# Kernel optimization log

Measured on AMD Instinct MI355X. Metric: run time of the kernel, lower is better.

The kernel has to match this reference:

```python
import jax, jax.numpy as jnp
import numpy as np
from jax import lax

B, S, C = 32, 64, 512      # batch, source length, context dim
E, H, L = 256, 512, 2      # embed dim, hidden dim, num GRU layers
V = 32000                  # vocab
START = 1                  # start token index


def setup_inputs() -> dict:
    key = jax.random.key(0)
    ks = jax.random.split(key, 16)
    s = 0.02
    d = {
        'context': jax.random.normal(ks[0], (B, S, C), jnp.float32),
        'max_len': 32,
        'embed': (jax.random.normal(ks[1], (V, E), jnp.float32) * s),
        'Wa': jax.random.normal(ks[2], (1, C + H), jnp.float32) * s,
        'ba': jnp.zeros((1,), jnp.float32),
        # GRU layer 0: input = E + C
        'W_ih0': jax.random.normal(ks[3], (3 * H, E + C), jnp.float32) * s,
        'W_hh0': jax.random.normal(ks[4], (3 * H, H), jnp.float32) * s,
        'b_ih0': jnp.zeros((3 * H,), jnp.float32),
        'b_hh0': jnp.zeros((3 * H,), jnp.float32),
        # GRU layer 1: input = H
        'W_ih1': jax.random.normal(ks[5], (3 * H, H), jnp.float32) * s,
        'W_hh1': jax.random.normal(ks[6], (3 * H, H), jnp.float32) * s,
        'b_ih1': jnp.zeros((3 * H,), jnp.float32),
        'b_hh1': jnp.zeros((3 * H,), jnp.float32),
        'Wo': jax.random.normal(ks[7], (V, H), jnp.float32) * s,
        'bo': jnp.zeros((V,), jnp.float32),
    }
    return d


def _gru_cell(x, h, Wih, Whh, bih, bhh):
    # PyTorch GRUCell math: gates order (r, z, n)
    gx = x @ Wih.T + bih
    gh = h @ Whh.T + bhh
    rx, zx, nx = jnp.split(gx, 3, axis=-1)
    rh, zh, nh = jnp.split(gh, 3, axis=-1)
    r = jax.nn.sigmoid(rx + rh)
    z = jax.nn.sigmoid(zx + zh)
    n = jnp.tanh(nx + r * nh)
    return (1.0 - z) * n + z * h


def reference(context, max_len, embed, Wa, ba,
              W_ih0, W_hh0, b_ih0, b_hh0,
              W_ih1, W_hh1, b_ih1, b_hh1,
              Wo, bo):
    def step(carry, _):
        x, hid = carry                      # x: [B] int32, hid: [L,B,H]
        ex = embed[x]                       # [B,E]
        htop = hid[L - 1]                   # [B,H] (top layer hidden)
        mem = jnp.broadcast_to(htop[:, None, :], (B, S, H))
        score = jnp.tanh(jnp.concatenate([mem, context], -1) @ Wa.T + ba)[..., 0]  # [B,S]
        w = jax.nn.softmax(score, axis=1)   # attention weights over source
        attend = jnp.einsum('bs,bsc->bc', w, context)  # [B,C]
        inp = jnp.concatenate([ex, attend], -1)        # [B,E+C]
        h0 = _gru_cell(inp, hid[0], W_ih0, W_hh0, b_ih0, b_hh0)
        h1 = _gru_cell(h0, hid[1], W_ih1, W_hh1, b_ih1, b_hh1)
        logp = jax.nn.log_softmax(h1 @ Wo.T + bo, axis=-1)  # [B,V]
        x_next = jnp.argmax(logp, axis=-1).astype(jnp.int32)  # greedy (detached)
        return (x_next, jnp.stack([h0, h1])), (logp, w)

    x0 = jnp.full((B,), START, jnp.int32)
    h0 = jnp.zeros((L, B, H), context.dtype)
    _, (outs, atts) = lax.scan(step, (x0, h0), None, length=max_len)
    out = jnp.transpose(outs, (1, 0, 2))        # [B,max_len,V]
    attention = jnp.transpose(atts, (1, 0, 2))  # [B,max_len,S]
    return out, attention
```

## Files before the change

kernel.cpp:

```cpp
#include <hip/hip_runtime.h>

#define B_ 32
#define S_ 64
#define C_ 512
#define E_ 256
#define H_ 512
#define V_ 32000
#define T_ 32
#define NTHR 512
#define ND 250
#define START_TOK 1
#define DELTA 0.05f
#define BH (B_ * H_)

#define OFF_CS   0
#define OFF_LSEA 2048
#define OFF_A2V  3072
#define OFF_A2I  527360
#define OFF_LSM  1051648
#define OFF_LSS  1313792
#define OFF_ATT  1575936
#define OFF_H0   1592320
#define OFF_H1   1625088
#define OFF_H1BF 1657856
#define OFF_WOBF 1920000
#define OFF_SYNC 10112000
#define WS_FLOATS 10113024

typedef unsigned long long ull;
typedef __attribute__((ext_vector_type(8))) short bf16x8;
typedef __attribute__((ext_vector_type(4))) float f32x4;

struct Params {
  const float* ctx; const float* embed; const float* Wa;
  const float* Wih0; const float* Whh0; const float* bih0; const float* bhh0;
  const float* Wih1; const float* Whh1; const float* bih1; const float* bhh1;
  const float* Wo; const float* bo;
  float* ws; float* out;
};

__device__ __forceinline__ float sigf(float x) { return 1.0f / (1.0f + expf(-x)); }

__device__ __forceinline__ unsigned short f2bf(float f) {
  unsigned u = __builtin_bit_cast(unsigned, f);
  unsigned r = (u + 0x7FFFu + ((u >> 16) & 1u)) >> 16;
  return (unsigned short)r;
}

__device__ __forceinline__ void lse_merge(float& m, float& s, float m2, float s2) {
  float M = fmaxf(m, m2);
  s = s * expf(m - M) + s2 * expf(m2 - M);
  m = M;
}

__device__ __forceinline__ void st_cf(float* p, float v) {
  __hip_atomic_store(p, v, __ATOMIC_RELAXED, __HIP_MEMORY_SCOPE_AGENT);
}
__device__ __forceinline__ unsigned ld_cu(const unsigned* p) {
  return __hip_atomic_load(p, __ATOMIC_RELAXED, __HIP_MEMORY_SCOPE_AGENT);
}

__global__ void __launch_bounds__(256) zero_k(float* wsf) {
  const unsigned i = blockIdx.x * 256u + threadIdx.x;
  if (i < 524288u) {
    wsf[OFF_A2V + i] = -3.0e38f;
    ((int*)wsf)[OFF_A2I + i] = 0x7fffffff;
  }
  if (i < 65536u) wsf[OFF_H0 + i] = 0.0f;
  if (i < 1024u) ((unsigned*)wsf)[OFF_SYNC + i] = 0u;
}

__global__ void __launch_bounds__(256) cscore_k(const float* __restrict__ ctx,
                                                const float* __restrict__ Wa,
                                                const float* __restrict__ ba,
                                                float* __restrict__ wsf) {
  const int b = blockIdx.x;
  const int s = threadIdx.x >> 2, q = threadIdx.x & 3;
  const float* cp = ctx + ((size_t)b * S_ + s) * C_ + q * 128;
  const float* wp = Wa + H_ + q * 128;
  float acc = 0.f;
#pragma unroll 8
  for (int k = 0; k < 128; ++k) acc = fmaf(cp[k], wp[k], acc);
  acc += __shfl_xor(acc, 1);
  acc += __shfl_xor(acc, 2);
  if (q == 0) wsf[OFF_CS + b * S_ + s] = acc + ba[0];
}

__global__ void __launch_bounds__(256) cvt_wobf(const float* __restrict__ wo,
                                                unsigned short* __restrict__ dst) {
  const size_t i = ((size_t)blockIdx.x * 256u + threadIdx.x) * 4;
  float4 v = *(const float4*)(wo + i);
  ushort4 o;
  o.x = f2bf(v.x); o.y = f2bf(v.y); o.z = f2bf(v.z); o.w = f2bf(v.w);
  *(ushort4*)(dst + i) = o;
}

__global__ void __launch_bounds__(NTHR) attn0_k(const float* __restrict__ ctx,
                                                float* __restrict__ wsf,
                                                float* __restrict__ out) {
  const int b = blockIdx.x, tx = threadIdx.x;
  __shared__ float wlds[S_];
  if (tx < S_) {
    float sc = tanhf(wsf[OFF_CS + b * S_ + tx]);
    float e = expf(sc); float sum = e;
#pragma unroll
    for (int d = 1; d < 64; d <<= 1) sum += __shfl_xor(sum, d);
    float w = e / sum; wlds[tx] = w;
    out[(size_t)B_ * T_ * V_ + ((size_t)b * T_ + 0) * S_ + tx] = w;
  }
  __syncthreads();
  float a0 = 0.f;
  const float* cb = ctx + (size_t)b * S_ * C_ + tx;
#pragma unroll 8
  for (int s2 = 0; s2 < S_; ++s2) a0 = fmaf(wlds[s2], cb[(size_t)s2 * C_], a0);
  wsf[OFF_ATT + (size_t)b * H_ + tx] = a0;
}

__global__ void __launch_bounds__(NTHR) k_gru01(Params p, int t) {
  float* wsf = p.ws;
  unsigned short* h1bf = (unsigned short*)(wsf + OFF_H1BF);
  const int bk = blockIdx.x, tx = threadIdx.x;
  const int ug = bk & 31, bg = bk >> 5, b4 = bg * 4;
  const int par = t & 1;
  __shared__ __align__(16) float sacts[4 * 768];
  __shared__ __align__(16) float sh0l[4 * 512];
  __shared__ __align__(16) float sh1r[4 * 512];
  __shared__ __align__(16) float sx[4 * 512];
  __shared__ int   stok4[4];
  __shared__ float scrV[8];
  __shared__ int   scrI[8];
  __shared__ float scrM[8];
  __shared__ int   slist4[4][16];
  __shared__ int   scnt4[4];
  __shared__ float hout[64];

  {
    const int bb = tx >> 7, cc = (tx & 127) * 4;
    float4 va = *(const float4*)(wsf + OFF_ATT + (size_t)(b4 + bb) * H_ + cc);
    float4 vh = *(const float4*)(wsf + OFF_H0 + (size_t)par * BH + (size_t)(b4 + bb) * H_ + cc);
    float4 vr = *(const float4*)(wsf + OFF_H1 + (size_t)par * BH + (size_t)(b4 + bb) * H_ + cc);
    *(float4*)&sacts[bb * 768 + 256 + cc] = va;
    *(float4*)&sh0l[bb * 512 + cc] = vh;
    *(float4*)&sh1r[bb * 512 + cc] = vr;
  }
  __syncthreads();
  if (t > 0) {
    const int w = tx >> 6, lane = tx & 63;
    const int lb = w >> 1, ws2 = w & 1, b = b4 + lb;
    const int gtx = tx & 127;
    const size_t cb_ = (size_t)(t - 1) * 32 + b;
    const float* avp = wsf + OFF_A2V + cb_ * 512;
    const int*   aip = (const int*)wsf + OFF_A2I + cb_ * 512;
    float v[4]; int id[4];
#pragma unroll
    for (int e = 0; e < 4; ++e) { v[e] = avp[gtx * 4 + e]; id[e] = aip[gtx * 4 + e]; }
    float M = fmaxf(fmaxf(v[0], v[1]), fmaxf(v[2], v[3]));
#pragma unroll
    for (int d = 1; d < 64; d <<= 1) M = fmaxf(M, __shfl_xor(M, d));
    if (lane == 0) scrM[w] = M;
    if (tx < 4) scnt4[tx] = 0;
    __syncthreads();
    M = fmaxf(scrM[lb * 2], scrM[lb * 2 + 1]);
#pragma unroll
    for (int e = 0; e < 4; ++e) {
      if (v[e] >= M - DELTA && id[e] != 0x7fffffff) {
        int k = atomicAdd(&scnt4[lb], 1);
        if (k < 16) slist4[lb][k] = id[e];
      }
    }
    __syncthreads();
    const int nc = min(scnt4[lb], 16);
    float bV = -3.0e38f; int bI = 0x7fffffff;
    for (int c = ws2; c < nc; c += 2) {
      const int idx = slist4[lb][c];
      const float* wr = p.Wo + (size_t)idx * H_ + lane * 8;
      const float* hr = sh1r + lb * 512 + lane * 8;
      float a = 0.f;
#pragma unroll
      for (int e = 0; e < 8; ++e) a = fmaf(hr[e], wr[e], a);
#pragma unroll
      for (int d = 1; d < 64; d <<= 1) a += __shfl_xor(a, d);
      a += p.bo[idx];
      if (a > bV || (a == bV && idx < bI)) { bV = a; bI = idx; }
    }
    if (lane == 0) { scrV[w] = bV; scrI[w] = bI; }
    __syncthreads();
    if (tx < 4) {
      float v0 = scrV[tx * 2], v1 = scrV[tx * 2 + 1];
      int i0 = scrI[tx * 2], i1 = scrI[tx * 2 + 1];
      stok4[tx] = (v1 > v0 || (v1 == v0 && i1 < i0)) ? i1 : i0;
    }
  } else {
    if (tx < 4) stok4[tx] = START_TOK;
  }
  __syncthreads();
#pragma unroll
  for (int k = 0; k < 2; ++k) {
    const int idx = k * NTHR + tx;
    const int bb = idx >> 8, e = idx & 255;
    sacts[bb * 768 + e] = p.embed[(size_t)stok4[bb] * E_ + e];
  }
  __syncthreads();
  const int u = tx >> 5, l = tx & 31;
  const int j = ug * 16 + u;
  {
    float red[16];
#pragma unroll
    for (int q = 0; q < 16; ++q) red[q] = 0.f;
#pragma unroll
    for (int g = 0; g < 3; ++g) {
      const float4* wx = (const float4*)(p.Wih0 + (size_t)(g * H_ + j) * 768);
      float* dx = (g < 2) ? &red[g * 4] : &red[8];
#pragma unroll
      for (int c = 0; c < 6; ++c) {
        float4 w = wx[l + 32 * c];
#pragma unroll
        for (int b2 = 0; b2 < 4; ++b2) {
          const float* a = &sacts[b2 * 768 + 4 * l + 128 * c];
          dx[b2] = fmaf(w.x, a[0], dx[b2]); dx[b2] = fmaf(w.y, a[1], dx[b2]);
          dx[b2] = fmaf(w.z, a[2], dx[b2]); dx[b2] = fmaf(w.w, a[3], dx[b2]);
        }
      }
      const float4* wh = (const float4*)(p.Whh0 + (size_t)(g * H_ + j) * H_);
      float* dh = (g < 2) ? &red[g * 4] : &red[12];
#pragma unroll
      for (int c = 0; c < 4; ++c) {
        float4 w = wh[l + 32 * c];
#pragma unroll
        for (int b2 = 0; b2 < 4; ++b2) {
          const float* a = &sh0l[b2 * 512 + 4 * l + 128 * c];
          dh[b2] = fmaf(w.x, a[0], dh[b2]); dh[b2] = fmaf(w.y, a[1], dh[b2]);
          dh[b2] = fmaf(w.z, a[2], dh[b2]); dh[b2] = fmaf(w.w, a[3], dh[b2]);
        }
      }
    }
#pragma unroll
    for (int d = 1; d < 32; d <<= 1)
#pragma unroll
      for (int q = 0; q < 16; ++q) red[q] += __shfl_xor(red[q], d);
    if (l < 4) {
      const float rr = sigf(red[l] + p.bih0[j] + p.bhh0[j]);
      const float zz = sigf(red[4 + l] + p.bih0[H_ + j] + p.bhh0[H_ + j]);
      const float nn = tanhf(red[8 + l] + p.bih0[2 * H_ + j] +
                             rr * (red[12 + l] + p.bhh0[2 * H_ + j]));
      const float hp = sh0l[l * 512 + j];
      st_cf(wsf + OFF_H0 + (size_t)(1 - par) * BH + (size_t)(b4 + l) * H_ + j,
            (1.f - zz) * nn + zz * hp);
    }
  }
  asm volatile("s_waitcnt vmcnt(0)" ::: "memory");
  __syncthreads();
  {
    unsigned* cnt = (unsigned*)wsf + OFF_SYNC + bg * 128 + t;
    if (tx == 0) {
      __hip_atomic_fetch_add(cnt, 1u, __ATOMIC_RELAXED, __HIP_MEMORY_SCOPE_AGENT);
      while (ld_cu(cnt) < 32u) __builtin_amdgcn_s_sleep(1);
    }
  }
  __syncthreads();
  {
    const ull* pX = (const ull*)(wsf + OFF_H0 + (size_t)(1 - par) * BH);
    ull vx[2];
#pragma unroll
    for (int k = 0; k < 2; ++k) {
      const int iu = k * NTHR + tx;
      const int bb = iu >> 8, cc = iu & 255;
      const ull* a1 = pX + (size_t)(b4 + bb) * 256 + cc;
      asm volatile("global_load_dwordx2 %0, %1, off sc0 sc1" : "=v"(vx[k]) : "v"(a1));
    }
    asm volatile("s_waitcnt vmcnt(0)" ::: "memory");
#pragma unroll
    for (int k = 0; k < 2; ++k) {
      const int iu = k * NTHR + tx;
      const int bb = iu >> 8, cc = iu & 255;
      *(ull*)&sx[bb * 512 + cc * 2] = vx[k];
    }
  }
  __syncthreads();
  {
    float red[16];
#pragma unroll
    for (int q = 0; q < 16; ++q) red[q] = 0.f;
#pragma unroll
    for (int g = 0; g < 3; ++g) {
      const float4* wx = (const float4*)(p.Wih1 + (size_t)(g * H_ + j) * H_);
      float* dx = (g < 2) ? &red[g * 4] : &red[8];
#pragma unroll
      for (int c = 0; c < 4; ++c) {
        float4 w = wx[l + 32 * c];
#pragma unroll
        for (int b2 = 0; b2 < 4; ++b2) {
          const float* a = &sx[b2 * 512 + 4 * l + 128 * c];
          dx[b2] = fmaf(w.x, a[0], dx[b2]); dx[b2] = fmaf(w.y, a[1], dx[b2]);
          dx[b2] = fmaf(w.z, a[2], dx[b2]); dx[b2] = fmaf(w.w, a[3], dx[b2]);
        }
      }
      const float4* wh = (const float4*)(p.Whh1 + (size_t)(g * H_ + j) * H_);
      float* dh = (g < 2) ? &red[g * 4] : &red[12];
#pragma unroll
      for (int c = 0; c < 4; ++c) {
        float4 w = wh[l + 32 * c];
#pragma unroll
        for (int b2 = 0; b2 < 4; ++b2) {
          const float* a = &sh1r[b2 * 512 + 4 * l + 128 * c];
          dh[b2] = fmaf(w.x, a[0], dh[b2]); dh[b2] = fmaf(w.y, a[1], dh[b2]);
          dh[b2] = fmaf(w.z, a[2], dh[b2]); dh[b2] = fmaf(w.w, a[3], dh[b2]);
        }
      }
    }
#pragma unroll
    for (int d = 1; d < 32; d <<= 1)
#pragma unroll
      for (int q = 0; q < 16; ++q) red[q] += __shfl_xor(red[q], d);
    if (l < 4) {
      const float rr = sigf(red[l] + p.bih1[j] + p.bhh1[j]);
      const float zz = sigf(red[4 + l] + p.bih1[H_ + j] + p.bhh1[H_ + j]);
      const float nn = tanhf(red[8 + l] + p.bih1[2 * H_ + j] +
                             rr * (red[12 + l] + p.bhh1[2 * H_ + j]));
      const float hp = sh1r[l * 512 + j];
      const float hnew = (1.f - zz) * nn + zz * hp;
      wsf[OFF_H1 + (size_t)(1 - par) * BH + (size_t)(b4 + l) * H_ + j] = hnew;
      hout[u * 4 + l] = hnew;
    }
  }
  __syncthreads();
  if (tx < 32) {
    const int b2 = tx & 3, pp = tx >> 2;
    const float h0v = hout[(pp * 2) * 4 + b2];
    const float h1v = hout[(pp * 2 + 1) * 4 + b2];
    const unsigned pk = (unsigned)f2bf(h0v) | ((unsigned)f2bf(h1v) << 16);
    *(int*)(h1bf + ((size_t)t * B_ + b4 + b2) * H_ + ug * 16 + pp * 2) = (int)pk;
  }
}

__device__ __constant__ int AST[7] = {0, 6, 12, 17, 22, 27, 32};

__global__ void __launch_bounds__(NTHR) k_scan(Params p, int t) {
  float* wsf = p.ws;
  const unsigned short* h1bf = (const unsigned short*)(wsf + OFF_H1BF);
  const unsigned short* wobf = (const unsigned short*)(wsf + OFF_WOBF);
  const int bk = blockIdx.x, tx = threadIdx.x;
  const int par = t & 1;
  __shared__ float scrF[8][16][4];
  __shared__ int   scrI2[8][16][2];
  __shared__ float wlds[S_];
  __shared__ float shsS;
  __shared__ float rv[NTHR];

  if (bk < ND) {
    const int v0 = bk * 128;
    const int w = tx >> 6, l = tx & 63, lr = l & 15, lq = l >> 4;
    const int vr = w * 16 + lr;
    const unsigned short* brow = wobf + (size_t)(v0 + vr) * H_ + lq * 8;
    for (int bt = 0; bt < 2; ++bt) {
      const unsigned short* arow = h1bf + ((size_t)t * B_ + bt * 16 + lr) * H_ + lq * 8;
      f32x4 acc = {0.f, 0.f, 0.f, 0.f};
#pragma unroll 4
      for (int kc = 0; kc < 16; ++kc) {
        bf16x8 a = *(const bf16x8*)(arow + kc * 32);
        bf16x8 bv = *(const bf16x8*)(brow + kc * 32);
        acc = __builtin_amdgcn_mfma_f32_16x16x32_bf16(a, bv, acc, 0, 0, 0);
      }
      const float bov = p.bo[v0 + vr];
#pragma unroll
      for (int r = 0; r < 4; ++r) {
        float v1 = acc[r] + bov, v2 = -3.0e38f;
        int i1 = v0 + vr, i2 = 0x7fffffff;
        float m = v1, s = 1.0f;
#pragma unroll
        for (int d = 1; d < 16; d <<= 1) {
          float w1 = __shfl_xor(v1, d); int j1 = __shfl_xor(i1, d);
          float w2 = __shfl_xor(v2, d); int j2 = __shfl_xor(i2, d);
          float m2 = __shfl_xor(m, d);  float s2 = __shfl_xor(s, d);
          if (w1 > v1 || (w1 == v1 && j1 < i1)) { v2 = v1; i2 = i1; v1 = w1; i1 = j1; }
          else if (w1 > v2 || (w1 == v2 && j1 < i2)) { v2 = w1; i2 = j1; }
          if (w2 > v2 || (w2 == v2 && j2 < i2)) {
            if (w2 > v1 || (w2 == v1 && j2 < i1)) { v2 = v1; i2 = i1; v1 = w2; i1 = j2; }
            else { v2 = w2; i2 = j2; }
          }
          lse_merge(m, s, m2, s2);
        }
        if (lr == 0) {
          const int bb = lq * 4 + r;
          scrF[w][bb][0] = v1; scrF[w][bb][1] = v2;
          scrF[w][bb][2] = m;  scrF[w][bb][3] = s;
          scrI2[w][bb][0] = i1; scrI2[w][bb][1] = i2;
        }
      }
      __syncthreads();
      if (tx < 16) {
        float v1 = scrF[0][tx][0], v2 = scrF[0][tx][1];
        float m = scrF[0][tx][2], s = scrF[0][tx][3];
        int i1 = scrI2[0][tx][0], i2 = scrI2[0][tx][1];
#pragma unroll
        for (int ww = 1; ww < 8; ++ww) {
          float w1 = scrF[ww][tx][0]; int j1 = scrI2[ww][tx][0];
          float w2 = scrF[ww][tx][1]; int j2 = scrI2[ww][tx][1];
          if (w1 > v1 || (w1 == v1 && j1 < i1)) { v2 = v1; i2 = i1; v1 = w1; i1 = j1; }
          else if (w1 > v2 || (w1 == v2 && j1 < i2)) { v2 = w1; i2 = j1; }
          if (w2 > v2 || (w2 == v2 && j2 < i2)) {
            if (w2 > v1 || (w2 == v1 && j2 < i1)) { v2 = v1; i2 = i1; v1 = w2; i1 = j2; }
            else { v2 = w2; i2 = j2; }
          }
          lse_merge(m, s, scrF[ww][tx][2], scrF[ww][tx][3]);
        }
        const int b = bt * 16 + tx;
        const size_t cb = (size_t)(t * 32 + b);
        wsf[OFF_LSM + cb * 256 + bk] = m;
        wsf[OFF_LSS + cb * 256 + bk] = s;
        wsf[OFF_A2V + cb * 512 + bk * 2] = v1;
        wsf[OFF_A2V + cb * 512 + bk * 2 + 1] = v2;
        ((int*)wsf)[OFF_A2I + cb * 512 + bk * 2] = i1;
        ((int*)wsf)[OFF_A2I + cb * 512 + bk * 2 + 1] = i2;
      }
      __syncthreads();
    }
  } else if (t < T_ - 1) {
    const int q = bk - ND;
    for (int b = AST[q]; b < AST[q + 1]; ++b) {
      const float h1v = wsf[OFF_H1 + (size_t)(1 - par) * BH + (size_t)b * H_ + tx];
      rv[tx] = h1v * p.Wa[tx];
      __syncthreads();
      if (tx < 64) {
        float v = 0.f;
#pragma unroll
        for (int o = 0; o < 8; ++o) v += rv[tx + o * 64];
#pragma unroll
        for (int d = 1; d < 64; d <<= 1) v += __shfl_xor(v, d);
        if (tx == 0) shsS = v;
      }
      __syncthreads();
      if (tx < S_) {
        float sc = tanhf(shsS + wsf[OFF_CS + b * S_ + tx]);
        float e = expf(sc); float sum = e;
#pragma unroll
        for (int d = 1; d < 64; d <<= 1) sum += __shfl_xor(sum, d);
        float w2 = e / sum; wlds[tx] = w2;
        p.out[(size_t)B_ * T_ * V_ + ((size_t)b * T_ + (t + 1)) * S_ + tx] = w2;
      }
      __syncthreads();
      float a0 = 0.f;
      const float* cb = p.ctx + (size_t)b * S_ * C_ + tx;
#pragma unroll 8
      for (int s2 = 0; s2 < S_; ++s2) a0 = fmaf(wlds[s2], cb[(size_t)s2 * C_], a0);
      wsf[OFF_ATT + (size_t)b * H_ + tx] = a0;
      __syncthreads();
    }
  }
}

__global__ void __launch_bounds__(256) lse_all(float* __restrict__ wsf) {
  const int id = blockIdx.x, tx = threadIdx.x;
  __shared__ float rm[256], rs[256];
  rm[tx] = (tx < ND) ? wsf[OFF_LSM + (size_t)id * 256 + tx] : -3.0e38f;
  rs[tx] = (tx < ND) ? wsf[OFF_LSS + (size_t)id * 256 + tx] : 0.f;
  __syncthreads();
  if (tx < 64) {
    float m = rm[tx], s = rs[tx];
#pragma unroll
    for (int o = 64; o < 256; o += 64) lse_merge(m, s, rm[tx + o], rs[tx + o]);
#pragma unroll
    for (int d = 1; d < 64; d <<= 1) {
      float m2 = __shfl_xor(m, d), s2 = __shfl_xor(s, d);
      lse_merge(m, s, m2, s2);
    }
    if (tx == 0) wsf[OFF_LSEA + id] = m + logf(s);
  }
}

__global__ void __launch_bounds__(NTHR) gemm_logp(const unsigned short* __restrict__ h1bf,
                                                  const unsigned short* __restrict__ wobf,
                                                  const float* __restrict__ bo,
                                                  const float* __restrict__ lsea,
                                                  float* __restrict__ out) {
  __shared__ __align__(16) unsigned short Bs[128 * 520];
  const int tx = threadIdx.x;
  const int v0 = blockIdx.x * 128;
  const int w = tx >> 6, l = tx & 63;
  const int lr = l & 15, lq = l >> 4;

#pragma unroll
  for (int e = 0; e < 16; ++e) {
    const int idx = e * NTHR + tx;
    const int row = idx >> 6, c = idx & 63;
    *(uint4*)&Bs[row * 520 + c * 8] = *(const uint4*)(wobf + (size_t)(v0 + row) * H_ + c * 8);
  }
  __syncthreads();

  float bov[8];
#pragma unroll
  for (int fn = 0; fn < 8; ++fn) bov[fn] = bo[v0 + fn * 16 + lr];

  for (int m0 = 0; m0 < 8; ++m0) {
    f32x4 acc[8];
#pragma unroll
    for (int fn = 0; fn < 8; ++fn) acc[fn] = (f32x4){0.f, 0.f, 0.f, 0.f};
    const unsigned short* arow = h1bf + (size_t)(m0 * 128 + w * 16 + lr) * H_ + lq * 8;
    bf16x8 a_cur = *(const bf16x8*)(arow);
#pragma unroll
    for (int kc = 0; kc < 16; ++kc) {
      bf16x8 a_nxt;
      if (kc < 15) a_nxt = *(const bf16x8*)(arow + (kc + 1) * 32);
#pragma unroll
      for (int fn = 0; fn < 8; ++fn) {
        bf16x8 bv = *(const bf16x8*)&Bs[(fn * 16 + lr) * 520 + lq * 8 + kc * 32];
        acc[fn] = __builtin_amdgcn_mfma_f32_16x16x32_bf16(a_cur, bv, acc[fn], 0, 0, 0);
      }
      a_cur = a_nxt;
    }
    float lse_r[4];
#pragma unroll
    for (int r = 0; r < 4; ++r) {
      const int M = m0 * 128 + w * 16 + lq * 4 + r;
      lse_r[r] = lsea[(M >> 5) * B_ + (M & 31)];
    }
#pragma unroll
    for (int fn = 0; fn < 8; ++fn) {
      const int v = v0 + fn * 16 + lr;
#pragma unroll
      for (int r = 0; r < 4; ++r) {
        const int M = m0 * 128 + w * 16 + lq * 4 + r;
        const int tt = M >> 5, b = M & 31;
        __builtin_nontemporal_store(acc[fn][r] + bov[fn] - lse_r[r],
                                    &out[((size_t)b * T_ + tt) * (size_t)V_ + v]);
      }
    }
  }
}

extern "C" void kernel_launch(void* const* d_in, const int* in_sizes, int n_in,
                              void* d_out, int out_size, void* d_ws, size_t ws_size,
                              hipStream_t stream) {
  (void)in_sizes; (void)n_in; (void)out_size;
  if (ws_size < (size_t)WS_FLOATS * sizeof(float)) return;

  const float* ctx   = (const float*)d_in[0];
  const float* embed = (const float*)d_in[2];
  const float* Wa    = (const float*)d_in[3];
  const float* ba    = (const float*)d_in[4];
  const float* Wih0  = (const float*)d_in[5];
  const float* Whh0  = (const float*)d_in[6];
  const float* bih0  = (const float*)d_in[7];
  const float* bhh0  = (const float*)d_in[8];
  const float* Wih1  = (const float*)d_in[9];
  const float* Whh1  = (const float*)d_in[10];
  const float* bih1  = (const float*)d_in[11];
  const float* bhh1  = (const float*)d_in[12];
  const float* Wo    = (const float*)d_in[13];
  const float* bo    = (const float*)d_in[14];
  float* ws  = (float*)d_ws;
  float* out = (float*)d_out;

  zero_k<<<dim3(2048), dim3(256), 0, stream>>>(ws);
  cscore_k<<<dim3(32), dim3(256), 0, stream>>>(ctx, Wa, ba, ws);
  cvt_wobf<<<dim3(16000), dim3(256), 0, stream>>>(Wo, (unsigned short*)(ws + OFF_WOBF));
  attn0_k<<<dim3(32), dim3(NTHR), 0, stream>>>(ctx, ws, out);

  Params p;
  p.ctx = ctx; p.embed = embed; p.Wa = Wa;
  p.Wih0 = Wih0; p.Whh0 = Whh0; p.bih0 = bih0; p.bhh0 = bhh0;
  p.Wih1 = Wih1; p.Whh1 = Whh1; p.bih1 = bih1; p.bhh1 = bhh1;
  p.Wo = Wo; p.bo = bo; p.ws = ws; p.out = out;

  for (int t = 0; t < T_; ++t) {
    k_gru01<<<dim3(256), dim3(NTHR), 0, stream>>>(p, t);
    k_scan<<<dim3(256), dim3(NTHR), 0, stream>>>(p, t);
  }

  lse_all<<<dim3(1024), dim3(256), 0, stream>>>(ws);
  gemm_logp<<<dim3(250), dim3(NTHR), 0, stream>>>(
      (const unsigned short*)(ws + OFF_H1BF), (const unsigned short*)(ws + OFF_WOBF),
      bo, ws + OFF_LSEA, out);
}
```

Measured before the change: 2.084 ms.

## Retile logits GEMM into 2D 128x128 blocks with double-buffered K staging

```diff
diff --git a/kernel.cpp b/kernel.cpp
--- a/kernel.cpp
+++ b/kernel.cpp
@@ -468,60 +468,65 @@
   }
 }
 
-__global__ void __launch_bounds__(NTHR) gemm_logp(const unsigned short* __restrict__ h1bf,
-                                                  const unsigned short* __restrict__ wobf,
-                                                  const float* __restrict__ bo,
-                                                  const float* __restrict__ lsea,
-                                                  float* __restrict__ out) {
-  __shared__ __align__(16) unsigned short Bs[128 * 520];
+__global__ void __launch_bounds__(256) gemm_logp(const unsigned short* __restrict__ h1bf,
+                                                 const unsigned short* __restrict__ wobf,
+                                                 const float* __restrict__ bo,
+                                                 const float* __restrict__ lsea,
+                                                 float* __restrict__ out) {
+  __shared__ __align__(16) unsigned short As[2][128 * 40];
+  __shared__ __align__(16) unsigned short Bs[2][128 * 40];
   const int tx = threadIdx.x;
-  const int v0 = blockIdx.x * 128;
+  const int v0 = blockIdx.x * 128, m0 = blockIdx.y * 128;
   const int w = tx >> 6, l = tx & 63;
+  const int wm = w >> 1, wn = w & 1;
+  f32x4 acc[4][4];
+#pragma unroll
+  for (int i = 0; i < 4; ++i)
+#pragma unroll
+    for (int j = 0; j < 4; ++j) acc[i][j] = (f32x4){0.f, 0.f, 0.f, 0.f};
+
+#define GSTAGE(ci, kc) {                                                        \
+    _Pragma("unroll")                                                           \
+    for (int e = 0; e < 2; ++e) {                                               \
+      const int seg = tx * 2 + e, row = seg >> 2, s = seg & 3;                  \
+      *(uint4*)&As[ci][row * 40 + s * 8] =                                      \
+          *(const uint4*)(h1bf + (size_t)(m0 + row) * H_ + (kc) * 32 + s * 8);  \
+      *(uint4*)&Bs[ci][row * 40 + s * 8] =                                      \
+          *(const uint4*)(wobf + (size_t)(v0 + row) * H_ + (kc) * 32 + s * 8);  \
+    } }
+
+  GSTAGE(0, 0);
+  __syncthreads();
+  for (int kc = 0; kc < 16; ++kc) {
+    const int cur = kc & 1;
+    if (kc < 15) GSTAGE(cur ^ 1, kc + 1);
+    const int lk = (l >> 4) * 8, lr = l & 15;
+    bf16x8 af[4], bf[4];
+#pragma unroll
+    for (int f = 0; f < 4; ++f) {
+      af[f] = *(const bf16x8*)&As[cur][(wm * 64 + f * 16 + lr) * 40 + lk];
+      bf[f] = *(const bf16x8*)&Bs[cur][(wn * 64 + f * 16 + lr) * 40 + lk];
+    }
+#pragma unroll
+    for (int fm = 0; fm < 4; ++fm)
+#pragma unroll
+      for (int fn = 0; fn < 4; ++fn)
+        acc[fm][fn] = __builtin_amdgcn_mfma_f32_16x16x32_bf16(af[fm], bf[fn], acc[fm][fn], 0, 0, 0);
+    __syncthreads();
+  }
+#undef GSTAGE
   const int lr = l & 15, lq = l >> 4;
-
-#pragma unroll
-  for (int e = 0; e < 16; ++e) {
-    const int idx = e * NTHR + tx;
-    const int row = idx >> 6, c = idx & 63;
-    *(uint4*)&Bs[row * 520 + c * 8] = *(const uint4*)(wobf + (size_t)(v0 + row) * H_ + c * 8);
-  }
-  __syncthreads();
-
-  float bov[8];
-#pragma unroll
-  for (int fn = 0; fn < 8; ++fn) bov[fn] = bo[v0 + fn * 16 + lr];
-
-  for (int m0 = 0; m0 < 8; ++m0) {
-    f32x4 acc[8];
-#pragma unroll
-    for (int fn = 0; fn < 8; ++fn) acc[fn] = (f32x4){0.f, 0.f, 0.f, 0.f};
-    const unsigned short* arow = h1bf + (size_t)(m0 * 128 + w * 16 + lr) * H_ + lq * 8;
-    bf16x8 a_cur = *(const bf16x8*)(arow);
-#pragma unroll
-    for (int kc = 0; kc < 16; ++kc) {
-      bf16x8 a_nxt;
-      if (kc < 15) a_nxt = *(const bf16x8*)(arow + (kc + 1) * 32);
-#pragma unroll
-      for (int fn = 0; fn < 8; ++fn) {
-        bf16x8 bv = *(const bf16x8*)&Bs[(fn * 16 + lr) * 520 + lq * 8 + kc * 32];
-        acc[fn] = __builtin_amdgcn_mfma_f32_16x16x32_bf16(a_cur, bv, acc[fn], 0, 0, 0);
-      }
-      a_cur = a_nxt;
-    }
-    float lse_r[4];
-#pragma unroll
-    for (int r = 0; r < 4; ++r) {
-      const int M = m0 * 128 + w * 16 + lq * 4 + r;
-      lse_r[r] = lsea[(M >> 5) * B_ + (M & 31)];
-    }
-#pragma unroll
-    for (int fn = 0; fn < 8; ++fn) {
-      const int v = v0 + fn * 16 + lr;
+#pragma unroll
+  for (int fm = 0; fm < 4; ++fm) {
+#pragma unroll
+    for (int fn = 0; fn < 4; ++fn) {
+      const int v = v0 + wn * 64 + fn * 16 + lr;
+      const float bov = bo[v];
 #pragma unroll
       for (int r = 0; r < 4; ++r) {
-        const int M = m0 * 128 + w * 16 + lq * 4 + r;
+        const int M = m0 + wm * 64 + fm * 16 + lq * 4 + r;
         const int tt = M >> 5, b = M & 31;
-        __builtin_nontemporal_store(acc[fn][r] + bov[fn] - lse_r[r],
+        __builtin_nontemporal_store(acc[fm][fn][r] + bov - lsea[tt * B_ + b],
                                     &out[((size_t)b * T_ + tt) * (size_t)V_ + v]);
       }
     }
@@ -568,7 +573,7 @@
   }
 
   lse_all<<<dim3(1024), dim3(256), 0, stream>>>(ws);
-  gemm_logp<<<dim3(250), dim3(NTHR), 0, stream>>>(
+  gemm_logp<<<dim3(250, 8), dim3(256), 0, stream>>>(
       (const unsigned short*)(ws + OFF_H1BF), (const unsigned short*)(ws + OFF_WOBF),
       bo, ws + OFF_LSEA, out);
 }
```

After: 1.903 ms. -8.7%, faster.
